# Kernel tuning notes

Measured on AMD Instinct MI355X. Metric: run time of the kernel, lower is better.

Reference implementation:

```python
import jax, jax.numpy as jnp
import numpy as np

B = 8388608  # batch of Euler-angle triples


def _euler_to_vec(angles):
    # angles: [B, 3] = (yaw, pitch, roll)
    # v = R_yaw @ R_pitch @ R_roll @ [0, 0, 1], expanded analytically:
    #   R_roll  @ e_z = [0, -sr, cr]
    #   R_pitch @ ... = [sp*cr, -sr, cp*cr]
    #   R_yaw   @ ... = [cy*sp*cr + sy*sr, sy*sp*cr - cy*sr, cp*cr]
    y, p, r = angles[:, 0], angles[:, 1], angles[:, 2]
    cy, sy = jnp.cos(y), jnp.sin(y)
    cp, sp = jnp.cos(p), jnp.sin(p)
    cr, sr = jnp.cos(r), jnp.sin(r)
    return jnp.stack([cy * sp * cr + sy * sr,
                      sy * sp * cr - cy * sr,
                      cp * cr], axis=-1)  # [B, 3]


def setup_inputs() -> dict:
    key = jax.random.key(0)
    k1, k2 = jax.random.split(key)
    output = jax.random.uniform(k1, (B, 3), dtype=jnp.float32)
    target = jax.random.uniform(k2, (B, 3), dtype=jnp.float32)
    return {"output": output, "target": target}


def reference(output, target):
    two_pi = 2.0 * jnp.pi
    out_ang = two_pi * (output - 0.5)
    tgt_ang = two_pi * (target - 0.5)
    vo = _euler_to_vec(out_ang)  # [B, 3]
    vt = _euler_to_vec(tgt_ang)  # [B, 3]
    cross = jnp.cross(vo, vt)                      # [B, 3]
    cross_norm = jnp.linalg.norm(cross, axis=-1)   # [B]
    dot = jnp.sum(vo * vt, axis=-1)                # [B]
    per_sample = 1.0 - cross_norm + dot
    return jnp.sum(per_sample)
```

## Files before the change

### kernel.cpp

```cpp
#include <hip/hip_runtime.h>
#include <math.h>


#define NBLOCKS 2048
#define NTHREADS 256

__device__ __forceinline__ float sample_loss(float a, float b, float c,
                                             float d, float e, float f) {
  float oy = a - 0.5f, op = b - 0.5f, orr = c - 0.5f;
  float ty = d - 0.5f, tp = e - 0.5f, trr = f - 0.5f;

  float cy = __builtin_amdgcn_cosf(oy), sy = __builtin_amdgcn_sinf(oy);
  float cp = __builtin_amdgcn_cosf(op), sp = __builtin_amdgcn_sinf(op);
  float cr = __builtin_amdgcn_cosf(orr), sr = __builtin_amdgcn_sinf(orr);

  float vox = cy * sp * cr + sy * sr;
  float voy = sy * sp * cr - cy * sr;
  float voz = cp * cr;

  float cy2 = __builtin_amdgcn_cosf(ty), sy2 = __builtin_amdgcn_sinf(ty);
  float cp2 = __builtin_amdgcn_cosf(tp), sp2 = __builtin_amdgcn_sinf(tp);
  float cr2 = __builtin_amdgcn_cosf(trr), sr2 = __builtin_amdgcn_sinf(trr);

  float vtx = cy2 * sp2 * cr2 + sy2 * sr2;
  float vty = sy2 * sp2 * cr2 - cy2 * sr2;
  float vtz = cp2 * cr2;

  float crx = voy * vtz - voz * vty;
  float cry = voz * vtx - vox * vtz;
  float crz = vox * vty - voy * vtx;

  float cn = sqrtf(crx * crx + cry * cry + crz * crz);
  float dot = vox * vtx + voy * vty + voz * vtz;
  return 1.0f - cn + dot;
}

__device__ __forceinline__ float block_reduce(float acc) {
  #pragma unroll
  for (int off = 32; off > 0; off >>= 1) acc += __shfl_down(acc, off, 64);
  __shared__ float ws[NTHREADS / 64];
  int lane = threadIdx.x & 63;
  int wave = threadIdx.x >> 6;
  if (lane == 0) ws[wave] = acc;
  __syncthreads();
  float tot = 0.0f;
  if (threadIdx.x == 0) {
    #pragma unroll
    for (int w = 0; w < NTHREADS / 64; ++w) tot += ws[w];
  }
  return tot;
}

__global__ __launch_bounds__(NTHREADS) void loss_partial_kernel(
    const float* __restrict__ out, const float* __restrict__ tgt,
    float* __restrict__ partial, int B) {
  const int tid = blockIdx.x * blockDim.x + threadIdx.x;
  const int nthreads = gridDim.x * blockDim.x;
  const int ngroups = B >> 2;

  const float4* __restrict__ o4 = (const float4*)out;
  const float4* __restrict__ t4 = (const float4*)tgt;

  float acc = 0.0f;
  for (int g = tid; g < ngroups; g += nthreads) {
    float4 o0 = o4[3 * g + 0];
    float4 o1 = o4[3 * g + 1];
    float4 o2 = o4[3 * g + 2];
    float4 t0 = t4[3 * g + 0];
    float4 t1 = t4[3 * g + 1];
    float4 t2 = t4[3 * g + 2];
    acc += sample_loss(o0.x, o0.y, o0.z, t0.x, t0.y, t0.z);
    acc += sample_loss(o0.w, o1.x, o1.y, t0.w, t1.x, t1.y);
    acc += sample_loss(o1.z, o1.w, o2.x, t1.z, t1.w, t2.x);
    acc += sample_loss(o2.y, o2.z, o2.w, t2.y, t2.z, t2.w);
  }
  for (int r = (ngroups << 2) + tid; r < B; r += nthreads) {
    acc += sample_loss(out[3 * r], out[3 * r + 1], out[3 * r + 2],
                       tgt[3 * r], tgt[3 * r + 1], tgt[3 * r + 2]);
  }

  float tot = block_reduce(acc);
  if (threadIdx.x == 0) partial[blockIdx.x] = tot;
}

__global__ __launch_bounds__(NTHREADS) void final_reduce_kernel(
    const float* __restrict__ partial, int n, float* __restrict__ out) {
  float acc = 0.0f;
  for (int i = threadIdx.x; i < n; i += NTHREADS) acc += partial[i];
  float tot = block_reduce(acc);
  if (threadIdx.x == 0) out[0] = tot;
}

extern "C" void kernel_launch(void* const* d_in, const int* in_sizes, int n_in,
                              void* d_out, int out_size, void* d_ws, size_t ws_size,
                              hipStream_t stream) {
  const float* d_output = (const float*)d_in[0];
  const float* d_target = (const float*)d_in[1];
  float* partial = (float*)d_ws;
  float* out = (float*)d_out;
  const int B = in_sizes[0] / 3;

  loss_partial_kernel<<<NBLOCKS, NTHREADS, 0, stream>>>(d_output, d_target,
                                                        partial, B);
  final_reduce_kernel<<<1, NTHREADS, 0, stream>>>(partial, NBLOCKS, out);
}
```

Baseline: 39.70 us.

## Stage tiles through LDS with register prefetch of next tile

```diff
diff --git a/kernel.cpp b/kernel.cpp
--- a/kernel.cpp
+++ b/kernel.cpp
@@ -2,8 +2,10 @@
 #include <math.h>
 
 
-#define NBLOCKS 2048
-#define NTHREADS 256
+#define NBLOCKS 1024
+#define NTHREADS 512
+#define TILE_ROWS 1024
+#define TILE_F2 (TILE_ROWS * 3 / 2)
 
 __device__ __forceinline__ float sample_loss(float a, float b, float c,
                                              float d, float e, float f) {
@@ -35,10 +37,11 @@
   return 1.0f - cn + dot;
 }
 
+template <int NT>
 __device__ __forceinline__ float block_reduce(float acc) {
   #pragma unroll
   for (int off = 32; off > 0; off >>= 1) acc += __shfl_down(acc, off, 64);
-  __shared__ float ws[NTHREADS / 64];
+  __shared__ float ws[NT / 64];
   int lane = threadIdx.x & 63;
   int wave = threadIdx.x >> 6;
   if (lane == 0) ws[wave] = acc;
@@ -46,7 +49,7 @@
   float tot = 0.0f;
   if (threadIdx.x == 0) {
     #pragma unroll
-    for (int w = 0; w < NTHREADS / 64; ++w) tot += ws[w];
+    for (int w = 0; w < NT / 64; ++w) tot += ws[w];
   }
   return tot;
 }
@@ -54,40 +57,65 @@
 __global__ __launch_bounds__(NTHREADS) void loss_partial_kernel(
     const float* __restrict__ out, const float* __restrict__ tgt,
     float* __restrict__ partial, int B) {
-  const int tid = blockIdx.x * blockDim.x + threadIdx.x;
-  const int nthreads = gridDim.x * blockDim.x;
-  const int ngroups = B >> 2;
+  __shared__ float2 ldsO2[TILE_F2];
+  __shared__ float2 ldsT2[TILE_F2];
+  const float* ldsO = (const float*)ldsO2;
+  const float* ldsT = (const float*)ldsT2;
 
-  const float4* __restrict__ o4 = (const float4*)out;
-  const float4* __restrict__ t4 = (const float4*)tgt;
+  const float2* __restrict__ o2 = (const float2*)out;
+  const float2* __restrict__ t2 = (const float2*)tgt;
+
+  const int t = threadIdx.x;
+  const int ntiles = B / TILE_ROWS;
 
   float acc = 0.0f;
-  for (int g = tid; g < ngroups; g += nthreads) {
-    float4 o0 = o4[3 * g + 0];
-    float4 o1 = o4[3 * g + 1];
-    float4 o2 = o4[3 * g + 2];
-    float4 t0 = t4[3 * g + 0];
-    float4 t1 = t4[3 * g + 1];
-    float4 t2 = t4[3 * g + 2];
-    acc += sample_loss(o0.x, o0.y, o0.z, t0.x, t0.y, t0.z);
-    acc += sample_loss(o0.w, o1.x, o1.y, t0.w, t1.x, t1.y);
-    acc += sample_loss(o1.z, o1.w, o2.x, t1.z, t1.w, t2.x);
-    acc += sample_loss(o2.y, o2.z, o2.w, t2.y, t2.z, t2.w);
+
+  int tile = blockIdx.x;
+  float2 a0, a1, a2, b0, b1, b2;
+  if (tile < ntiles) {
+    const int g = tile * TILE_F2 + t;
+    a0 = o2[g]; a1 = o2[g + NTHREADS]; a2 = o2[g + 2 * NTHREADS];
+    b0 = t2[g]; b1 = t2[g + NTHREADS]; b2 = t2[g + 2 * NTHREADS];
   }
-  for (int r = (ngroups << 2) + tid; r < B; r += nthreads) {
+
+  while (tile < ntiles) {
+    ldsO2[t] = a0; ldsO2[t + NTHREADS] = a1; ldsO2[t + 2 * NTHREADS] = a2;
+    ldsT2[t] = b0; ldsT2[t + NTHREADS] = b1; ldsT2[t + 2 * NTHREADS] = b2;
+    __syncthreads();
+
+    const int next = tile + gridDim.x;
+    if (next < ntiles) {
+      const int g = next * TILE_F2 + t;
+      a0 = o2[g]; a1 = o2[g + NTHREADS]; a2 = o2[g + 2 * NTHREADS];
+      b0 = t2[g]; b1 = t2[g + NTHREADS]; b2 = t2[g + 2 * NTHREADS];
+    }
+
+    #pragma unroll
+    for (int k = 0; k < TILE_ROWS / NTHREADS; ++k) {
+      const int r = t + k * NTHREADS;
+      acc += sample_loss(ldsO[3 * r], ldsO[3 * r + 1], ldsO[3 * r + 2],
+                         ldsT[3 * r], ldsT[3 * r + 1], ldsT[3 * r + 2]);
+    }
+    __syncthreads();
+    tile = next;
+  }
+
+  const int done = ntiles * TILE_ROWS;
+  for (int r = done + blockIdx.x * NTHREADS + t; r < B;
+       r += gridDim.x * NTHREADS) {
     acc += sample_loss(out[3 * r], out[3 * r + 1], out[3 * r + 2],
                        tgt[3 * r], tgt[3 * r + 1], tgt[3 * r + 2]);
   }
 
-  float tot = block_reduce(acc);
-  if (threadIdx.x == 0) partial[blockIdx.x] = tot;
+  float tot = block_reduce<NTHREADS>(acc);
+  if (t == 0) partial[blockIdx.x] = tot;
 }
 
-__global__ __launch_bounds__(NTHREADS) void final_reduce_kernel(
+__global__ __launch_bounds__(256) void final_reduce_kernel(
     const float* __restrict__ partial, int n, float* __restrict__ out) {
   float acc = 0.0f;
-  for (int i = threadIdx.x; i < n; i += NTHREADS) acc += partial[i];
-  float tot = block_reduce(acc);
+  for (int i = threadIdx.x; i < n; i += 256) acc += partial[i];
+  float tot = block_reduce<256>(acc);
   if (threadIdx.x == 0) out[0] = tot;
 }
 
@@ -102,5 +130,5 @@
 
   loss_partial_kernel<<<NBLOCKS, NTHREADS, 0, stream>>>(d_output, d_target,
                                                         partial, B);
-  final_reduce_kernel<<<1, NTHREADS, 0, stream>>>(partial, NBLOCKS, out);
+  final_reduce_kernel<<<1, 256, 0, stream>>>(partial, NBLOCKS, out);
 }
```

After: 38.26 us, median of 2. 1.04x faster.
